# Optimization experiments

Measured on AMD Instinct MI355X. Metric: run time of the kernel, lower is better.

## Reference

```python
import jax, jax.numpy as jnp
import numpy as np

# --- config (matches init_kwargs) ---
E = 32          # n_routed_experts
G = 8           # n_group
TKG = 4         # topk_group
K = 4           # num_experts_per_tok
D = 2048        # hidden_size
H = 1024        # moe_intermediate_size
HS = 4096       # moe_shared_expert_intermediate_size
SCALE = 2.5     # routed_scaling_factor
CAP = 1024


def setup_inputs() -> dict:
    key = jax.random.key(0)
    ks = jax.random.split(key, 6)
    B, S = 2, 2048
    return dict(
        hidden_states=jax.random.normal(ks[0], (B, S, D), jnp.float32),
        gate_w=jax.random.normal(ks[1], (E, D), jnp.float32) * 0.02,
        bias_corr=jnp.zeros((E,), jnp.float32),  # e_score_correction_bias
        up_w=jax.random.normal(ks[2], (E, H, D), jnp.float32) * 0.02,
        down_w=jax.random.normal(ks[3], (E, D, H), jnp.float32) * 0.02,
        shared_up_w=jax.random.normal(ks[4], (HS, D), jnp.float32) * 0.02,
        shared_down_w=jax.random.normal(ks[5], (D, HS), jnp.float32) * 0.02,
    )


def relu2(x):
    r = jnp.maximum(x, 0.0)
    return r * r


def route_tokens(scores, bias_corr):
    # scores: sigmoid(router_logits), [T, E]
    T = scores.shape[0]
    scores_c = scores + bias_corr                                  # for choice
    group_scores = jax.lax.top_k(scores_c.reshape(T, G, E // G), 2)[0].sum(-1)  # [T, G]
    _, group_idx = jax.lax.top_k(group_scores, TKG)                # [T, TKG]
    group_mask = jnp.zeros((T, G), scores.dtype).at[jnp.arange(T)[:, None], group_idx].set(1.0)
    score_mask = jnp.repeat(group_mask, E // G, axis=1)            # [T, E]
    masked = jnp.where(score_mask > 0, scores_c, 0.0)
    _, topk_idx = jax.lax.top_k(masked, K)                         # [T, K]
    topk_w = jnp.take_along_axis(scores, topk_idx, axis=1)         # weights from raw sigmoid scores
    topk_w = topk_w / (topk_w.sum(-1, keepdims=True) + 1e-20)      # norm_topk_prob
    return topk_idx, topk_w * SCALE


def reference(hidden_states, gate_w, bias_corr, up_w, down_w, shared_up_w, shared_down_w):
    B, S, _ = hidden_states.shape
    T = B * S
    flat = hidden_states.reshape(T, D)

    logits = flat @ gate_w.T                                       # [T, E]
    scores = jax.nn.sigmoid(logits)
    topk_idx, topk_w = route_tokens(scores, bias_corr)             # [T, K] each

    # --- capacity-based dispatch (equivalent to per-expert gather + index_add combine) ---
    e_flat = topk_idx.reshape(-1)                                  # [T*K]
    oh = jax.nn.one_hot(e_flat, E, dtype=jnp.int32)                # [T*K, E]
    pos = jnp.take_along_axis(jnp.cumsum(oh, axis=0) - 1, e_flat[:, None], axis=1)[:, 0]
    tok = jnp.repeat(jnp.arange(T), K)                             # token idx per assignment
    valid = pos < CAP

    xe = jnp.zeros((E, CAP, D), flat.dtype).at[e_flat, pos].set(flat[tok], mode='drop')
    h = relu2(jnp.einsum('ecd,ehd->ech', xe, up_w))                # [E, CAP, H]
    ye = jnp.einsum('ech,edh->ecd', h, down_w)                     # [E, CAP, D]

    gathered = ye[e_flat, jnp.minimum(pos, CAP - 1)]               # [T*K, D]
    gathered = jnp.where(valid[:, None], gathered, 0.0) * topk_w.reshape(-1)[:, None]
    routed = gathered.reshape(T, K, D).sum(axis=1).reshape(B, S, D)

    shared = relu2(hidden_states @ shared_up_w.T) @ shared_down_w.T
    return routed + shared
```

## Files before the change

### kernel.cpp

```cpp
#include <hip/hip_runtime.h>

#define NE 32
#define NG 8
#define NK 4
#define ND 2048
#define NH 1024
#define NHS 4096
#define CAPE 1024
#define NT 4096

typedef float f32x4 __attribute__((ext_vector_type(4)));
typedef short s16x8 __attribute__((ext_vector_type(8)));

__device__ __forceinline__ short f2bf(float f) {
    return __builtin_bit_cast(short, (__bf16)f);
}
__device__ __forceinline__ float bf2f(short h) {
    return __builtin_bit_cast(float, ((unsigned)(unsigned short)h) << 16);
}

__device__ __forceinline__ void gload_lds16(const void* g, void* l) {
    __builtin_amdgcn_global_load_lds(
        (const __attribute__((address_space(1))) void*)g,
        (__attribute__((address_space(3))) void*)l, 16, 0, 0);
}

__global__ __launch_bounds__(256) void gate_kernel(
    const float* __restrict__ X, const float* __restrict__ Gw,
    const float* __restrict__ bias,
    int* __restrict__ topk_idx, float* __restrict__ topk_w)
{
    const int lane = threadIdx.x & 63;
    const int t = blockIdx.x * 4 + (threadIdx.x >> 6);
    const float* x = X + (size_t)t * ND;

    float xr[32];
#pragma unroll
    for (int i = 0; i < 32; i++) xr[i] = x[lane + i * 64];

    float scores[32];
#pragma unroll
    for (int e = 0; e < 32; e++) {
        const float* w = Gw + (size_t)e * ND;
        float a = 0.f;
#pragma unroll
        for (int i = 0; i < 32; i++) a = fmaf(xr[i], w[lane + i * 64], a);
#pragma unroll
        for (int s = 32; s > 0; s >>= 1) a += __shfl_xor(a, s);
        scores[e] = 1.0f / (1.0f + expf(-a));
    }

    float sc_c[32];
#pragma unroll
    for (int e = 0; e < 32; e++) sc_c[e] = scores[e] + bias[e];

    float gs[8];
#pragma unroll
    for (int g = 0; g < 8; g++) {
        float a = sc_c[4 * g], b = sc_c[4 * g + 1], c = sc_c[4 * g + 2], d = sc_c[4 * g + 3];
        float hi1 = fmaxf(a, b), lo1 = fminf(a, b);
        float hi2 = fmaxf(c, d), lo2 = fminf(c, d);
        float m1 = fmaxf(hi1, hi2);
        float m2 = fmaxf(fminf(hi1, hi2), fmaxf(lo1, lo2));
        gs[g] = m1 + m2;
    }

    unsigned gsel = 0;
#pragma unroll
    for (int it = 0; it < 4; it++) {
        int best = -1; float bv = -1e30f;
#pragma unroll
        for (int g = 0; g < 8; g++) {
            bool avail = !((gsel >> g) & 1);
            if (avail && gs[g] > bv) { bv = gs[g]; best = g; }
        }
        gsel |= 1u << best;
    }

    unsigned esel = 0;
    int idxs[4]; float wts[4];
#pragma unroll
    for (int it = 0; it < 4; it++) {
        int best = -1; float bv = -1e30f, braw = 0.f;
#pragma unroll
        for (int e = 0; e < 32; e++) {
            float mv = ((gsel >> (e >> 2)) & 1) ? sc_c[e] : 0.0f;
            bool avail = !((esel >> e) & 1);
            if (avail && mv > bv) { bv = mv; best = e; braw = scores[e]; }
        }
        esel |= 1u << best;
        idxs[it] = best; wts[it] = braw;
    }

    float s = wts[0] + wts[1] + wts[2] + wts[3] + 1e-20f;
    if (lane == 0) {
#pragma unroll
        for (int k = 0; k < 4; k++) {
            topk_idx[t * 4 + k] = idxs[k];
            topk_w[t * 4 + k] = wts[k] / s * 2.5f;
        }
    }
}

__global__ void zero_cnt(int* cnt) {
    if (threadIdx.x < NE) cnt[threadIdx.x] = 0;
}

__global__ void dispatch_kernel(const int* __restrict__ topk_idx,
                                int* __restrict__ cnt,
                                int* __restrict__ tok_list,
                                int* __restrict__ pos_list)
{
    int i = blockIdx.x * 256 + threadIdx.x;
    int e = topk_idx[i];
    int t = i >> 2;
    int pos = atomicAdd(&cnt[e], 1);
    pos_list[i] = pos;
    if (pos < CAPE) {
        tok_list[e * CAPE + pos] = t;
    }
}

__global__ __launch_bounds__(256) void cvt_f2bf(const float* __restrict__ in,
                                                short* __restrict__ out, int n8)
{
    int i = blockIdx.x * 256 + threadIdx.x;
    int stride = gridDim.x * 256;
    for (; i < n8; i += stride) {
        const f32x4* p = (const f32x4*)(in + (size_t)i * 8);
        f32x4 a = p[0], b = p[1];
        s16x8 h;
        h[0] = f2bf(a[0]); h[1] = f2bf(a[1]); h[2] = f2bf(a[2]); h[3] = f2bf(a[3]);
        h[4] = f2bf(b[0]); h[5] = f2bf(b[1]); h[6] = f2bf(b[2]); h[7] = f2bf(b[3]);
        *(s16x8*)(out + (size_t)i * 8) = h;
    }
}

__global__ __launch_bounds__(256) void combine_kernel(
    const int* __restrict__ topk_idx, const float* __restrict__ topk_w,
    const int* __restrict__ pos_list,
    const short* __restrict__ Ybuf, float* __restrict__ out)
{
    const int t = blockIdx.x;
    const int d0 = threadIdx.x * 8;

    int e[NK], p[NK]; float w[NK];
#pragma unroll
    for (int k = 0; k < NK; k++) {
        e[k] = topk_idx[t * NK + k];
        p[k] = pos_list[t * NK + k];
        w[k] = topk_w[t * NK + k];
    }

    float* orow = out + (size_t)t * ND + d0;
    f32x4 o0 = *(f32x4*)(orow);
    f32x4 o1 = *(f32x4*)(orow + 4);

#pragma unroll
    for (int k = 0; k < NK; k++) {
        if (p[k] < CAPE) {
            s16x8 y = *(const s16x8*)(Ybuf + ((size_t)e[k] * CAPE + p[k]) * ND + d0);
            o0[0] = fmaf(w[k], bf2f(y[0]), o0[0]);
            o0[1] = fmaf(w[k], bf2f(y[1]), o0[1]);
            o0[2] = fmaf(w[k], bf2f(y[2]), o0[2]);
            o0[3] = fmaf(w[k], bf2f(y[3]), o0[3]);
            o1[0] = fmaf(w[k], bf2f(y[4]), o1[0]);
            o1[1] = fmaf(w[k], bf2f(y[5]), o1[1]);
            o1[2] = fmaf(w[k], bf2f(y[6]), o1[2]);
            o1[3] = fmaf(w[k], bf2f(y[7]), o1[3]);
        }
    }
    *(f32x4*)(orow) = o0;
    *(f32x4*)(orow + 4) = o1;
}

template <int MODE>
__global__ __launch_bounds__(256, 2) void moe_gemm4(
    const short* __restrict__ Abase, const float* __restrict__ Bbase,
    const int* __restrict__ cnt, const int* __restrict__ tok_list,
    short* __restrict__ Hout, float* __restrict__ out)
{
    constexpr int K = (MODE == 0) ? ND : (MODE == 1) ? NH : (MODE == 2) ? ND : NHS;
    constexpr int NTILES = K / 64;

    const int e = blockIdx.z;
    const int m0 = blockIdx.y * 128, n0 = blockIdx.x * 128;

    int mcnt = 0;
    if constexpr (MODE == 0 || MODE == 1) {
        mcnt = min(cnt[e], CAPE);
        if (m0 >= mcnt) return;
    }

    __shared__ short As[2][128 * 64];
    __shared__ short Bs[2][128 * 64];

    const int tid = threadIdx.x;
    const int lane = tid & 63;
    const int wave = tid >> 6;
    const int wr = wave >> 1, wc = wave & 1;

    const short* Ab = Abase;
    const float* Bb = Bbase;
    if constexpr (MODE == 0) Bb += (size_t)e * NH * ND;
    if constexpr (MODE == 1) { Ab += (size_t)e * CAPE * NH; Bb += (size_t)e * ND * NH; }

    const int srow = tid >> 3;
    const int pA = tid & 7;
    const int gcolA = (pA ^ (srow & 7)) * 8;
    const short* asrc[4];
    int dstA[4];
#pragma unroll
    for (int o = 0; o < 4; o++) {
        int r = o * 32 + srow;
        if constexpr (MODE == 0) {
            int gr = min(m0 + r, mcnt - 1);
            int tok = tok_list[e * CAPE + gr];
            asrc[o] = Abase + (size_t)tok * ND + gcolA;
        } else if constexpr (MODE == 1) {
            int gr = min(m0 + r, mcnt - 1);
            asrc[o] = Ab + (size_t)gr * NH + gcolA;
        } else if constexpr (MODE == 2) {
            asrc[o] = Abase + (size_t)(m0 + r) * ND + gcolA;
        } else {
            asrc[o] = Abase + (size_t)(m0 + r) * NHS + gcolA;
        }
        dstA[o] = o * 2048 + wave * 512;
    }

    const int brow = tid >> 4;
    const int lc = tid & 15;
    const float* bsrc[8];
    int bdst[8];
#pragma unroll
    for (int o = 0; o < 8; o++) {
        int r = o * 16 + brow;
        bsrc[o] = Bb + (size_t)(n0 + r) * K + lc * 4;
        int ks = lc >> 1;
        bdst[o] = r * 64 + ((ks ^ (r & 7)) * 8) + (lc & 1) * 4;
    }

    auto STAGE_A = [&](int tt, int par) {
        const int ko = (tt < NTILES ? tt : NTILES - 1) * 64;
        short* Ad = As[par];
#pragma unroll
        for (int o = 0; o < 4; o++) gload_lds16(asrc[o] + ko, Ad + dstA[o]);
    };
    auto BLOAD = [&](int tt, f32x4* regs) {
        const int ko = (tt < NTILES ? tt : NTILES - 1) * 64;
#pragma unroll
        for (int o = 0; o < 8; o++) regs[o] = *(const f32x4*)(bsrc[o] + ko);
    };
    auto BWRITE = [&](const f32x4* regs, int par) {
        short* Bd = Bs[par];
#pragma unroll
        for (int o = 0; o < 8; o++) {
            short4 h;
            h.x = f2bf(regs[o][0]); h.y = f2bf(regs[o][1]);
            h.z = f2bf(regs[o][2]); h.w = f2bf(regs[o][3]);
            *(short4*)(Bd + bdst[o]) = h;
        }
    };

    const int r16 = lane & 15;
    const int physbase = ((lane >> 4) ^ (lane & 7)) * 8;
    int offA[4], offB[4];
#pragma unroll
    for (int m = 0; m < 4; m++)
        offA[m] = (wr * 64 + m * 16 + r16) * 64 + physbase;
#pragma unroll
    for (int n = 0; n < 4; n++)
        offB[n] = (wc * 64 + n * 16 + r16) * 64 + physbase;

    f32x4 acc[4][4] = {};
    f32x4 brE[8], brO[8];

    STAGE_A(0, 0); STAGE_A(1, 1);
    BLOAD(0, brE); BLOAD(1, brO);
    asm volatile("s_waitcnt vmcnt(8)" ::: "memory");
    __builtin_amdgcn_sched_barrier(0);
    BWRITE(brE, 0);
    asm volatile("s_waitcnt vmcnt(0)" ::: "memory");
    __builtin_amdgcn_sched_barrier(0);
    BWRITE(brO, 1);
    BLOAD(2, brE);
    asm volatile("s_waitcnt lgkmcnt(0)" ::: "memory");
    __builtin_amdgcn_sched_barrier(0);

#define GEMM_ITER(T, PAR, CONSUME, FILL)                                        \
    {                                                                           \
        __builtin_amdgcn_s_barrier();                                           \
        __builtin_amdgcn_sched_barrier(0);                                      \
        const short* At = As[PAR];                                              \
        const short* Bt = Bs[PAR];                                              \
        s16x8 af[4], bf[4];                                                     \
        _Pragma("unroll")                                                       \
        for (int m = 0; m < 4; m++) af[m] = *(const s16x8*)(At + offA[m]);      \
        _Pragma("unroll")                                                       \
        for (int n = 0; n < 4; n++) bf[n] = *(const s16x8*)(Bt + offB[n]);      \
        asm volatile("s_waitcnt lgkmcnt(0)" ::: "memory");                      \
        __builtin_amdgcn_sched_barrier(0);                                      \
        __builtin_amdgcn_s_setprio(1);                                          \
        _Pragma("unroll")                                                       \
        for (int m = 0; m < 4; m++)                                             \
            _Pragma("unroll")                                                   \
            for (int n = 0; n < 4; n++)                                         \
                acc[m][n] = __builtin_amdgcn_mfma_f32_16x16x32_bf16(            \
                    af[m], bf[n], acc[m][n], 0, 0, 0);                          \
        __builtin_amdgcn_s_setprio(0);                                          \
        s16x8 ag[4], bg[4];                                                     \
        _Pragma("unroll")                                                       \
        for (int m = 0; m < 4; m++) ag[m] = *(const s16x8*)(At + (offA[m] ^ 32)); \
        _Pragma("unroll")                                                       \
        for (int n = 0; n < 4; n++) bg[n] = *(const s16x8*)(Bt + (offB[n] ^ 32)); \
        asm volatile("s_waitcnt lgkmcnt(0)" ::: "memory");                      \
        __builtin_amdgcn_sched_barrier(0);                                      \
        __builtin_amdgcn_s_barrier();         \
        __builtin_amdgcn_sched_barrier(0);                                      \
        STAGE_A((T) + 2, PAR);                                                  \
        BLOAD((T) + 3, FILL);                                                   \
        asm volatile("s_waitcnt vmcnt(12)" ::: "memory");  \
        __builtin_amdgcn_sched_barrier(0);                                      \
        BWRITE(CONSUME, PAR);                                                   \
        __builtin_amdgcn_s_setprio(1);                                          \
        _Pragma("unroll")                                                       \
        for (int m = 0; m < 4; m++)                                             \
            _Pragma("unroll")                                                   \
            for (int n = 0; n < 4; n++)                                         \
                acc[m][n] = __builtin_amdgcn_mfma_f32_16x16x32_bf16(            \
                    ag[m], bg[n], acc[m][n], 0, 0, 0);                          \
        __builtin_amdgcn_s_setprio(0);                                          \
        asm volatile("s_waitcnt lgkmcnt(0)" ::: "memory");                      \
        __builtin_amdgcn_sched_barrier(0);                                      \
    }

    for (int t = 0; t < NTILES; t += 2) {
        GEMM_ITER(t,     0, brE, brO);
        GEMM_ITER(t + 1, 1, brO, brE);
    }
#undef GEMM_ITER

    const int r0 = (lane >> 4) * 4;
    const int cc = lane & 15;

    if constexpr (MODE == 0 || MODE == 2) {
#pragma unroll
        for (int i = 0; i < 4; i++)
#pragma unroll
            for (int j = 0; j < 4; j++)
#pragma unroll
                for (int v = 0; v < 4; v++) {
                    int row = wr * 64 + i * 16 + r0 + v;
                    int col = wc * 64 + j * 16 + cc;
                    float val = acc[i][j][v];
                    float r = fmaxf(val, 0.f);
                    val = r * r;
                    if constexpr (MODE == 0)
                        Hout[((size_t)e * CAPE + m0 + row) * NH + (n0 + col)] = f2bf(val);
                    else
                        Hout[(size_t)(m0 + row) * NHS + (n0 + col)] = f2bf(val);
                }
    } else if constexpr (MODE == 3) {
#pragma unroll
        for (int i = 0; i < 4; i++)
#pragma unroll
            for (int j = 0; j < 4; j++)
#pragma unroll
                for (int v = 0; v < 4; v++) {
                    int row = wr * 64 + i * 16 + r0 + v;
                    int col = wc * 64 + j * 16 + cc;
                    out[(size_t)(m0 + row) * ND + (n0 + col)] = acc[i][j][v];
                }
    } else {
#pragma unroll
        for (int i = 0; i < 4; i++)
#pragma unroll
            for (int v = 0; v < 4; v++) {
                int row = wr * 64 + i * 16 + r0 + v;
                int grow = m0 + row;
                if (grow < mcnt) {
#pragma unroll
                    for (int j = 0; j < 4; j++) {
                        int col = wc * 64 + j * 16 + cc;
                        Hout[((size_t)e * CAPE + grow) * ND + (n0 + col)] = f2bf(acc[i][j][v]);
                    }
                }
            }
    }
}

extern "C" void kernel_launch(void* const* d_in, const int* in_sizes, int n_in,
                              void* d_out, int out_size, void* d_ws, size_t ws_size,
                              hipStream_t stream) {
    const float* X    = (const float*)d_in[0];
    const float* Gw   = (const float*)d_in[1];
    const float* bias = (const float*)d_in[2];
    const float* up_w = (const float*)d_in[3];
    const float* dn_w = (const float*)d_in[4];
    const float* sup  = (const float*)d_in[5];
    const float* sdn  = (const float*)d_in[6];
    float* out = (float*)d_out;

    char* ws = (char*)d_ws;
    size_t off = 0;
    auto alloc = [&](size_t bytes) -> void* {
        off = (off + 255) & ~(size_t)255;
        void* p = ws + off;
        off += bytes;
        return p;
    };
    int*   cnt      = (int*)  alloc(NE * 4);
    int*   topk_idx = (int*)  alloc((size_t)NT * NK * 4);
    float* topk_w   = (float*)alloc((size_t)NT * NK * 4);
    int*   pos_list = (int*)  alloc((size_t)NT * NK * 4);
    int*   tok_list = (int*)  alloc((size_t)NE * CAPE * 4);
    short* Hbuf     = (short*)alloc((size_t)NE * CAPE * NH * 2);
    short* Sbuf     = (short*)alloc((size_t)NT * NHS * 2);
    short* Xbf      = (short*)alloc((size_t)NT * ND * 2);
    short* Ybuf     = (short*)alloc((size_t)NE * CAPE * ND * 2);

    gate_kernel<<<dim3(NT / 4), dim3(256), 0, stream>>>(X, Gw, bias, topk_idx, topk_w);
    zero_cnt<<<dim3(1), dim3(64), 0, stream>>>(cnt);
    dispatch_kernel<<<dim3(NT * NK / 256), dim3(256), 0, stream>>>(
        topk_idx, cnt, tok_list, pos_list);

    cvt_f2bf<<<dim3(1024), dim3(256), 0, stream>>>(X, Xbf, NT * ND / 8);

    moe_gemm4<0><<<dim3(NH / 128, CAPE / 128, NE), dim3(256), 0, stream>>>(
        Xbf, up_w, cnt, tok_list, Hbuf, nullptr);
    moe_gemm4<2><<<dim3(NHS / 128, NT / 128, 1), dim3(256), 0, stream>>>(
        Xbf, sup, nullptr, nullptr, Sbuf, nullptr);
    moe_gemm4<3><<<dim3(ND / 128, NT / 128, 1), dim3(256), 0, stream>>>(
        Sbuf, sdn, nullptr, nullptr, nullptr, out);
    moe_gemm4<1><<<dim3(ND / 128, CAPE / 128, NE), dim3(256), 0, stream>>>(
        Hbuf, dn_w, cnt, tok_list, Ybuf, nullptr);
    combine_kernel<<<dim3(NT), dim3(256), 0, stream>>>(
        topk_idx, topk_w, pos_list, Ybuf, out);
}
```

Baseline: 645.0 us.

## Restructure GEMM to K=32 tiles with 4-stage A pipeline and 3 blocks/CU

Rewrites the bf16 MFMA GEMM main loop to use 32-wide K tiles. A now streams through a 4-deep LDS ring and B is register-prefetched four tiles ahead and converted into a double-buffered LDS slot. Shrinking LDS per block and raising launch bounds to 3 blocks per SM is meant to increase occupancy and hide global load latency. The trade-off is twice as many barriers per K, fewer MFMAs between syncs, and added register pressure from four B register sets under a tighter VGPR budget.

Result: slower. 779.9 us (+20.9%).

```diff
diff --git a/kernel.cpp b/kernel.cpp
--- a/kernel.cpp
+++ b/kernel.cpp
@@ -175,13 +175,13 @@
 }
 
 template <int MODE>
-__global__ __launch_bounds__(256, 2) void moe_gemm4(
+__global__ __launch_bounds__(256, 3) void moe_gemm5(
     const short* __restrict__ Abase, const float* __restrict__ Bbase,
     const int* __restrict__ cnt, const int* __restrict__ tok_list,
     short* __restrict__ Hout, float* __restrict__ out)
 {
     constexpr int K = (MODE == 0) ? ND : (MODE == 1) ? NH : (MODE == 2) ? ND : NHS;
-    constexpr int NTILES = K / 64;
+    constexpr int NTILES = K / 32;
 
     const int e = blockIdx.z;
     const int m0 = blockIdx.y * 128, n0 = blockIdx.x * 128;
@@ -192,8 +192,8 @@
         if (m0 >= mcnt) return;
     }
 
-    __shared__ short As[2][128 * 64];
-    __shared__ short Bs[2][128 * 64];
+    __shared__ short As[4][128 * 32];
+    __shared__ short Bs[2][128 * 32];
 
     const int tid = threadIdx.x;
     const int lane = tid & 63;
@@ -205,14 +205,14 @@
     if constexpr (MODE == 0) Bb += (size_t)e * NH * ND;
     if constexpr (MODE == 1) { Ab += (size_t)e * CAPE * NH; Bb += (size_t)e * ND * NH; }
 
-    const int srow = tid >> 3;
-    const int pA = tid & 7;
-    const int gcolA = (pA ^ (srow & 7)) * 8;
-    const short* asrc[4];
-    int dstA[4];
-#pragma unroll
-    for (int o = 0; o < 4; o++) {
-        int r = o * 32 + srow;
+    const int arow = tid >> 2;
+    const int aslot = tid & 3;
+    const int gcolA = (aslot ^ (arow & 3)) * 8;
+    const short* asrc[2];
+    int dstA[2];
+#pragma unroll
+    for (int o = 0; o < 2; o++) {
+        int r = o * 64 + arow;
         if constexpr (MODE == 0) {
             int gr = min(m0 + r, mcnt - 1);
             int tok = tok_list[e * CAPE + gr];
@@ -228,71 +228,73 @@
         dstA[o] = o * 2048 + wave * 512;
     }
 
-    const int brow = tid >> 4;
-    const int lc = tid & 15;
-    const float* bsrc[8];
-    int bdst[8];
-#pragma unroll
-    for (int o = 0; o < 8; o++) {
-        int r = o * 16 + brow;
-        bsrc[o] = Bb + (size_t)(n0 + r) * K + lc * 4;
-        int ks = lc >> 1;
-        bdst[o] = r * 64 + ((ks ^ (r & 7)) * 8) + (lc & 1) * 4;
-    }
-
-    auto STAGE_A = [&](int tt, int par) {
-        const int ko = (tt < NTILES ? tt : NTILES - 1) * 64;
-        short* Ad = As[par];
-#pragma unroll
-        for (int o = 0; o < 4; o++) gload_lds16(asrc[o] + ko, Ad + dstA[o]);
+    const int brow = tid >> 1;
+    const int bhalf = tid & 1;
+    const float* bsrcp = Bb + (size_t)(n0 + brow) * K + bhalf * 16;
+    const int bd0 = brow * 32 + (((2 * bhalf)     ^ (brow & 3)) * 8);
+    const int bd1 = brow * 32 + (((2 * bhalf + 1) ^ (brow & 3)) * 8);
+
+    auto STAGE_A = [&](int tt) {
+        const int ko = (tt < NTILES ? tt : NTILES - 1) * 32;
+        short* Ad = As[tt & 3];
+#pragma unroll
+        for (int o = 0; o < 2; o++) gload_lds16(asrc[o] + ko, Ad + dstA[o]);
     };
     auto BLOAD = [&](int tt, f32x4* regs) {
-        const int ko = (tt < NTILES ? tt : NTILES - 1) * 64;
-#pragma unroll
-        for (int o = 0; o < 8; o++) regs[o] = *(const f32x4*)(bsrc[o] + ko);
+        const int ko = (tt < NTILES ? tt : NTILES - 1) * 32;
+#pragma unroll
+        for (int i = 0; i < 4; i++) regs[i] = *(const f32x4*)(bsrcp + ko + i * 4);
     };
     auto BWRITE = [&](const f32x4* regs, int par) {
         short* Bd = Bs[par];
-#pragma unroll
-        for (int o = 0; o < 8; o++) {
-            short4 h;
-            h.x = f2bf(regs[o][0]); h.y = f2bf(regs[o][1]);
-            h.z = f2bf(regs[o][2]); h.w = f2bf(regs[o][3]);
-            *(short4*)(Bd + bdst[o]) = h;
-        }
+        s16x8 h0, h1;
+        h0[0] = f2bf(regs[0][0]); h0[1] = f2bf(regs[0][1]);
+        h0[2] = f2bf(regs[0][2]); h0[3] = f2bf(regs[0][3]);
+        h0[4] = f2bf(regs[1][0]); h0[5] = f2bf(regs[1][1]);
+        h0[6] = f2bf(regs[1][2]); h0[7] = f2bf(regs[1][3]);
+        h1[0] = f2bf(regs[2][0]); h1[1] = f2bf(regs[2][1]);
+        h1[2] = f2bf(regs[2][2]); h1[3] = f2bf(regs[2][3]);
+        h1[4] = f2bf(regs[3][0]); h1[5] = f2bf(regs[3][1]);
+        h1[6] = f2bf(regs[3][2]); h1[7] = f2bf(regs[3][3]);
+        *(s16x8*)(Bd + bd0) = h0;
+        *(s16x8*)(Bd + bd1) = h1;
     };
 
     const int r16 = lane & 15;
-    const int physbase = ((lane >> 4) ^ (lane & 7)) * 8;
+    const int ks = lane >> 4;
+    const int physA = (ks ^ (r16 & 3)) * 8;
     int offA[4], offB[4];
 #pragma unroll
     for (int m = 0; m < 4; m++)
-        offA[m] = (wr * 64 + m * 16 + r16) * 64 + physbase;
+        offA[m] = (wr * 64 + m * 16 + r16) * 32 + physA;
 #pragma unroll
     for (int n = 0; n < 4; n++)
-        offB[n] = (wc * 64 + n * 16 + r16) * 64 + physbase;
+        offB[n] = (wc * 64 + n * 16 + r16) * 32 + physA;
 
     f32x4 acc[4][4] = {};
-    f32x4 brE[8], brO[8];
-
-    STAGE_A(0, 0); STAGE_A(1, 1);
-    BLOAD(0, brE); BLOAD(1, brO);
-    asm volatile("s_waitcnt vmcnt(8)" ::: "memory");
+    f32x4 br0[4], br1[4], br2[4], br3[4];
+
+    STAGE_A(0); BLOAD(0, br0);
+    BLOAD(1, br1); STAGE_A(1);
+    BLOAD(2, br2); STAGE_A(2);
+    BLOAD(3, br3);
+    asm volatile("s_waitcnt vmcnt(16)" ::: "memory");
     __builtin_amdgcn_sched_barrier(0);
-    BWRITE(brE, 0);
-    asm volatile("s_waitcnt vmcnt(0)" ::: "memory");
-    __builtin_amdgcn_sched_barrier(0);
-    BWRITE(brO, 1);
-    BLOAD(2, brE);
+    BWRITE(br0, 0);
     asm volatile("s_waitcnt lgkmcnt(0)" ::: "memory");
     __builtin_amdgcn_sched_barrier(0);
 
-#define GEMM_ITER(T, PAR, CONSUME, FILL)                                        \
+#define GEMM_ITER(T, BRW, BRL)                                                  \
     {                                                                           \
         __builtin_amdgcn_s_barrier();                                           \
         __builtin_amdgcn_sched_barrier(0);                                      \
-        const short* At = As[PAR];                                              \
-        const short* Bt = Bs[PAR];                                              \
+        STAGE_A((T) + 3);                                                       \
+        asm volatile("s_waitcnt vmcnt(12)" ::: "memory");                       \
+        __builtin_amdgcn_sched_barrier(0);                                      \
+        BWRITE(BRW, ((T) + 1) & 1);                                             \
+        BLOAD((T) + 4, BRL);                                                    \
+        const short* At = As[(T) & 3];                                          \
+        const short* Bt = Bs[(T) & 1];                                          \
         s16x8 af[4], bf[4];                                                     \
         _Pragma("unroll")                                                       \
         for (int m = 0; m < 4; m++) af[m] = *(const s16x8*)(At + offA[m]);      \
@@ -308,35 +310,13 @@
                 acc[m][n] = __builtin_amdgcn_mfma_f32_16x16x32_bf16(            \
                     af[m], bf[n], acc[m][n], 0, 0, 0);                          \
         __builtin_amdgcn_s_setprio(0);                                          \
-        s16x8 ag[4], bg[4];                                                     \
-        _Pragma("unroll")                                                       \
-        for (int m = 0; m < 4; m++) ag[m] = *(const s16x8*)(At + (offA[m] ^ 32)); \
-        _Pragma("unroll")                                                       \
-        for (int n = 0; n < 4; n++) bg[n] = *(const s16x8*)(Bt + (offB[n] ^ 32)); \
-        asm volatile("s_waitcnt lgkmcnt(0)" ::: "memory");                      \
-        __builtin_amdgcn_sched_barrier(0);                                      \
-        __builtin_amdgcn_s_barrier();         \
-        __builtin_amdgcn_sched_barrier(0);                                      \
-        STAGE_A((T) + 2, PAR);                                                  \
-        BLOAD((T) + 3, FILL);                                                   \
-        asm volatile("s_waitcnt vmcnt(12)" ::: "memory");  \
-        __builtin_amdgcn_sched_barrier(0);                                      \
-        BWRITE(CONSUME, PAR);                                                   \
-        __builtin_amdgcn_s_setprio(1);                                          \
-        _Pragma("unroll")                                                       \
-        for (int m = 0; m < 4; m++)                                             \
-            _Pragma("unroll")                                                   \
-            for (int n = 0; n < 4; n++)                                         \
-                acc[m][n] = __builtin_amdgcn_mfma_f32_16x16x32_bf16(            \
-                    ag[m], bg[n], acc[m][n], 0, 0, 0);                          \
-        __builtin_amdgcn_s_setprio(0);                                          \
-        asm volatile("s_waitcnt lgkmcnt(0)" ::: "memory");                      \
-        __builtin_amdgcn_sched_barrier(0);                                      \
-    }
-
-    for (int t = 0; t < NTILES; t += 2) {
-        GEMM_ITER(t,     0, brE, brO);
-        GEMM_ITER(t + 1, 1, brO, brE);
+    }
+
+    for (int t = 0; t < NTILES; t += 4) {
+        GEMM_ITER(t + 0, br1, br0);
+        GEMM_ITER(t + 1, br2, br1);
+        GEMM_ITER(t + 2, br3, br2);
+        GEMM_ITER(t + 3, br0, br3);
     }
 #undef GEMM_ITER
 
@@ -426,13 +406,13 @@
 
     cvt_f2bf<<<dim3(1024), dim3(256), 0, stream>>>(X, Xbf, NT * ND / 8);
 
-    moe_gemm4<0><<<dim3(NH / 128, CAPE / 128, NE), dim3(256), 0, stream>>>(
+    moe_gemm5<0><<<dim3(NH / 128, CAPE / 128, NE), dim3(256), 0, stream>>>(
         Xbf, up_w, cnt, tok_list, Hbuf, nullptr);
-    moe_gemm4<2><<<dim3(NHS / 128, NT / 128, 1), dim3(256), 0, stream>>>(
+    moe_gemm5<2><<<dim3(NHS / 128, NT / 128, 1), dim3(256), 0, stream>>>(
         Xbf, sup, nullptr, nullptr, Sbuf, nullptr);
-    moe_gemm4<3><<<dim3(ND / 128, NT / 128, 1), dim3(256), 0, stream>>>(
+    moe_gemm5<3><<<dim3(ND / 128, NT / 128, 1), dim3(256), 0, stream>>>(
         Sbuf, sdn, nullptr, nullptr, nullptr, out);
-    moe_gemm4<1><<<dim3(ND / 128, CAPE / 128, NE), dim3(256), 0, stream>>>(
+    moe_gemm5<1><<<dim3(ND / 128, CAPE / 128, NE), dim3(256), 0, stream>>>(
         Hbuf, dn_w, cnt, tok_list, Ybuf, nullptr);
     combine_kernel<<<dim3(NT), dim3(256), 0, stream>>>(
         topk_idx, topk_w, pos_list, Ybuf, out);
```

## Merge routed and shared GEMMs into combined up/down launches, fold counter zeroing

Applied to the files above, without the earlier changes.

Replaces the four templated GEMM launches with two grouped kernels: one runs the routed expert up-projections and the shared up-projection in a single grid, the other runs the routed and shared down-projections. The counter zeroing moves into the gate kernel, and the B-tile global load is issued at the start of each pipeline iteration instead of after the A staging. The intent is to cut launch count and tail idle time and to let shared-expert tiles fill CUs left empty by skipped routed tiles. In exchange, K and the routed/shared choice become runtime values, which may cost registers or unrolling, and the cnt reset relies on the gate kernel finishing before dispatch.

Measured after the change: 638.9 us, median of 3. About the same (-0.9%).

```diff
diff --git a/kernel.cpp b/kernel.cpp
--- a/kernel.cpp
+++ b/kernel.cpp
@@ -28,8 +28,11 @@
 __global__ __launch_bounds__(256) void gate_kernel(
     const float* __restrict__ X, const float* __restrict__ Gw,
     const float* __restrict__ bias,
-    int* __restrict__ topk_idx, float* __restrict__ topk_w)
+    int* __restrict__ topk_idx, float* __restrict__ topk_w,
+    int* __restrict__ cnt)
 {
+    if (blockIdx.x == 0 && threadIdx.x < NE) cnt[threadIdx.x] = 0;
+
     const int lane = threadIdx.x & 63;
     const int t = blockIdx.x * 4 + (threadIdx.x >> 6);
     const float* x = X + (size_t)t * ND;
@@ -100,10 +103,6 @@
             topk_w[t * 4 + k] = wts[k] / s * 2.5f;
         }
     }
-}
-
-__global__ void zero_cnt(int* cnt) {
-    if (threadIdx.x < NE) cnt[threadIdx.x] = 0;
 }
 
 __global__ void dispatch_kernel(const int* __restrict__ topk_idx,
@@ -174,123 +173,31 @@
     *(f32x4*)(orow + 4) = o1;
 }
 
-template <int MODE>
-__global__ __launch_bounds__(256, 2) void moe_gemm4(
-    const short* __restrict__ Abase, const float* __restrict__ Bbase,
-    const int* __restrict__ cnt, const int* __restrict__ tok_list,
-    short* __restrict__ Hout, float* __restrict__ out)
-{
-    constexpr int K = (MODE == 0) ? ND : (MODE == 1) ? NH : (MODE == 2) ? ND : NHS;
-    constexpr int NTILES = K / 64;
-
-    const int e = blockIdx.z;
-    const int m0 = blockIdx.y * 128, n0 = blockIdx.x * 128;
-
-    int mcnt = 0;
-    if constexpr (MODE == 0 || MODE == 1) {
-        mcnt = min(cnt[e], CAPE);
-        if (m0 >= mcnt) return;
-    }
-
-    __shared__ short As[2][128 * 64];
-    __shared__ short Bs[2][128 * 64];
-
-    const int tid = threadIdx.x;
-    const int lane = tid & 63;
-    const int wave = tid >> 6;
-    const int wr = wave >> 1, wc = wave & 1;
-
-    const short* Ab = Abase;
-    const float* Bb = Bbase;
-    if constexpr (MODE == 0) Bb += (size_t)e * NH * ND;
-    if constexpr (MODE == 1) { Ab += (size_t)e * CAPE * NH; Bb += (size_t)e * ND * NH; }
-
-    const int srow = tid >> 3;
-    const int pA = tid & 7;
-    const int gcolA = (pA ^ (srow & 7)) * 8;
-    const short* asrc[4];
-    int dstA[4];
-#pragma unroll
-    for (int o = 0; o < 4; o++) {
-        int r = o * 32 + srow;
-        if constexpr (MODE == 0) {
-            int gr = min(m0 + r, mcnt - 1);
-            int tok = tok_list[e * CAPE + gr];
-            asrc[o] = Abase + (size_t)tok * ND + gcolA;
-        } else if constexpr (MODE == 1) {
-            int gr = min(m0 + r, mcnt - 1);
-            asrc[o] = Ab + (size_t)gr * NH + gcolA;
-        } else if constexpr (MODE == 2) {
-            asrc[o] = Abase + (size_t)(m0 + r) * ND + gcolA;
-        } else {
-            asrc[o] = Abase + (size_t)(m0 + r) * NHS + gcolA;
-        }
-        dstA[o] = o * 2048 + wave * 512;
-    }
-
-    const int brow = tid >> 4;
-    const int lc = tid & 15;
-    const float* bsrc[8];
-    int bdst[8];
-#pragma unroll
-    for (int o = 0; o < 8; o++) {
-        int r = o * 16 + brow;
-        bsrc[o] = Bb + (size_t)(n0 + r) * K + lc * 4;
-        int ks = lc >> 1;
-        bdst[o] = r * 64 + ((ks ^ (r & 7)) * 8) + (lc & 1) * 4;
-    }
-
-    auto STAGE_A = [&](int tt, int par) {
-        const int ko = (tt < NTILES ? tt : NTILES - 1) * 64;
-        short* Ad = As[par];
-#pragma unroll
-        for (int o = 0; o < 4; o++) gload_lds16(asrc[o] + ko, Ad + dstA[o]);
-    };
-    auto BLOAD = [&](int tt, f32x4* regs) {
-        const int ko = (tt < NTILES ? tt : NTILES - 1) * 64;
-#pragma unroll
-        for (int o = 0; o < 8; o++) regs[o] = *(const f32x4*)(bsrc[o] + ko);
-    };
-    auto BWRITE = [&](const f32x4* regs, int par) {
-        short* Bd = Bs[par];
-#pragma unroll
-        for (int o = 0; o < 8; o++) {
-            short4 h;
-            h.x = f2bf(regs[o][0]); h.y = f2bf(regs[o][1]);
-            h.z = f2bf(regs[o][2]); h.w = f2bf(regs[o][3]);
-            *(short4*)(Bd + bdst[o]) = h;
-        }
-    };
-
-    const int r16 = lane & 15;
-    const int physbase = ((lane >> 4) ^ (lane & 7)) * 8;
-    int offA[4], offB[4];
-#pragma unroll
-    for (int m = 0; m < 4; m++)
-        offA[m] = (wr * 64 + m * 16 + r16) * 64 + physbase;
-#pragma unroll
-    for (int n = 0; n < 4; n++)
-        offB[n] = (wc * 64 + n * 16 + r16) * 64 + physbase;
-
-    f32x4 acc[4][4] = {};
-    f32x4 brE[8], brO[8];
-
-    STAGE_A(0, 0); STAGE_A(1, 1);
-    BLOAD(0, brE); BLOAD(1, brO);
-    asm volatile("s_waitcnt vmcnt(8)" ::: "memory");
-    __builtin_amdgcn_sched_barrier(0);
-    BWRITE(brE, 0);
-    asm volatile("s_waitcnt vmcnt(0)" ::: "memory");
-    __builtin_amdgcn_sched_barrier(0);
-    BWRITE(brO, 1);
-    BLOAD(2, brE);
-    asm volatile("s_waitcnt lgkmcnt(0)" ::: "memory");
-    __builtin_amdgcn_sched_barrier(0);
+#define GEMM_BODY_SETUP()                                                       \
+    __shared__ short As[2][128 * 64];                                           \
+    __shared__ short Bs[2][128 * 64];                                           \
+    const int tid = threadIdx.x;                                                \
+    const int lane = tid & 63;                                                  \
+    const int wave = tid >> 6;                                                  \
+    const int wr = wave >> 1, wc = wave & 1;                                    \
+    const int srow = tid >> 3;                                                  \
+    const int pA = tid & 7;                                                     \
+    const int gcolA = (pA ^ (srow & 7)) * 8;                                    \
+    const int brow = tid >> 4;                                                  \
+    const int lc = tid & 15;                                                    \
+    const int r16 = lane & 15;                                                  \
+    const int physbase = ((lane >> 4) ^ (lane & 7)) * 8;                        \
+    int offA[4], offB[4];                                                       \
+    _Pragma("unroll")                                                           \
+    for (int m = 0; m < 4; m++) offA[m] = (wr * 64 + m * 16 + r16) * 64 + physbase; \
+    _Pragma("unroll")                                                           \
+    for (int n = 0; n < 4; n++) offB[n] = (wc * 64 + n * 16 + r16) * 64 + physbase;
 
 #define GEMM_ITER(T, PAR, CONSUME, FILL)                                        \
     {                                                                           \
         __builtin_amdgcn_s_barrier();                                           \
         __builtin_amdgcn_sched_barrier(0);                                      \
+        BLOAD((T) + 3, FILL);                                                   \
         const short* At = As[PAR];                                              \
         const short* Bt = Bs[PAR];                                              \
         s16x8 af[4], bf[4];                                                     \
@@ -318,10 +225,9 @@
         __builtin_amdgcn_s_barrier();         \
         __builtin_amdgcn_sched_barrier(0);                                      \
         STAGE_A((T) + 2, PAR);                                                  \
-        BLOAD((T) + 3, FILL);                                                   \
         asm volatile("s_waitcnt vmcnt(12)" ::: "memory");  \
         __builtin_amdgcn_sched_barrier(0);                                      \
-        BWRITE(CONSUME, PAR);                                                   \
+        BWRITE(CONSUME, PAR);                            \
         __builtin_amdgcn_s_setprio(1);                                          \
         _Pragma("unroll")                                                       \
         for (int m = 0; m < 4; m++)                                             \
@@ -334,33 +240,227 @@
         __builtin_amdgcn_sched_barrier(0);                                      \
     }
 
+#define GEMM_PROLOGUE()                                                         \
+    STAGE_A(0, 0); STAGE_A(1, 1);                                               \
+    BLOAD(0, brE); BLOAD(1, brO);                                               \
+    asm volatile("s_waitcnt vmcnt(8)" ::: "memory");                            \
+    __builtin_amdgcn_sched_barrier(0);                                          \
+    BWRITE(brE, 0);                                                             \
+    asm volatile("s_waitcnt vmcnt(0)" ::: "memory");                            \
+    __builtin_amdgcn_sched_barrier(0);                                          \
+    BWRITE(brO, 1);                                                             \
+    BLOAD(2, brE);                                                              \
+    asm volatile("s_waitcnt lgkmcnt(0)" ::: "memory");                          \
+    __builtin_amdgcn_sched_barrier(0);
+
+__global__ __launch_bounds__(256, 2) void fused_up(
+    const short* __restrict__ Xbf, const float* __restrict__ up_w,
+    const float* __restrict__ sup,
+    const int* __restrict__ cnt, const int* __restrict__ tok_list,
+    short* __restrict__ Hbuf, short* __restrict__ Sbuf)
+{
+    constexpr int K = ND;
+    constexpr int NTILES = K / 64;
+
+    const int bid = blockIdx.x;
+    const bool routed = bid < 2048;
+    int e = 0, m0, n0, mcnt = 0;
+    const float* Bb;
+    if (routed) {
+        e = bid >> 6;
+        m0 = ((bid >> 3) & 7) * 128;
+        n0 = (bid & 7) * 128;
+        mcnt = min(cnt[e], CAPE);
+        if (m0 >= mcnt) return;
+        Bb = up_w + (size_t)e * NH * ND;
+    } else {
+        int lin = bid - 2048;
+        m0 = (lin >> 5) * 128;
+        n0 = (lin & 31) * 128;
+        Bb = sup;
+    }
+
+    GEMM_BODY_SETUP();
+
+    const short* asrc[4];
+    int dstA[4];
+#pragma unroll
+    for (int o = 0; o < 4; o++) {
+        int r = o * 32 + srow;
+        int arow;
+        if (routed) {
+            int gr = min(m0 + r, mcnt - 1);
+            arow = tok_list[e * CAPE + gr];
+        } else {
+            arow = m0 + r;
+        }
+        asrc[o] = Xbf + (size_t)arow * ND + gcolA;
+        dstA[o] = o * 2048 + wave * 512;
+    }
+
+    const float* bsrc[8];
+    int bdst[8];
+#pragma unroll
+    for (int o = 0; o < 8; o++) {
+        int r = o * 16 + brow;
+        bsrc[o] = Bb + (size_t)(n0 + r) * K + lc * 4;
+        int ks = lc >> 1;
+        bdst[o] = r * 64 + ((ks ^ (r & 7)) * 8) + (lc & 1) * 4;
+    }
+
+    auto STAGE_A = [&](int tt, int par) {
+        const int ko = (tt < NTILES ? tt : NTILES - 1) * 64;
+        short* Ad = As[par];
+#pragma unroll
+        for (int o = 0; o < 4; o++) gload_lds16(asrc[o] + ko, Ad + dstA[o]);
+    };
+    auto BLOAD = [&](int tt, f32x4* regs) {
+        const int ko = (tt < NTILES ? tt : NTILES - 1) * 64;
+#pragma unroll
+        for (int o = 0; o < 8; o++) regs[o] = *(const f32x4*)(bsrc[o] + ko);
+    };
+    auto BWRITE = [&](const f32x4* regs, int par) {
+        short* Bd = Bs[par];
+#pragma unroll
+        for (int o = 0; o < 8; o++) {
+            short4 h;
+            h.x = f2bf(regs[o][0]); h.y = f2bf(regs[o][1]);
+            h.z = f2bf(regs[o][2]); h.w = f2bf(regs[o][3]);
+            *(short4*)(Bd + bdst[o]) = h;
+        }
+    };
+
+    f32x4 acc[4][4] = {};
+    f32x4 brE[8], brO[8];
+
+    GEMM_PROLOGUE();
     for (int t = 0; t < NTILES; t += 2) {
         GEMM_ITER(t,     0, brE, brO);
         GEMM_ITER(t + 1, 1, brO, brE);
     }
-#undef GEMM_ITER
 
     const int r0 = (lane >> 4) * 4;
     const int cc = lane & 15;
-
-    if constexpr (MODE == 0 || MODE == 2) {
+#pragma unroll
+    for (int i = 0; i < 4; i++)
+#pragma unroll
+        for (int j = 0; j < 4; j++)
+#pragma unroll
+            for (int v = 0; v < 4; v++) {
+                int row = wr * 64 + i * 16 + r0 + v;
+                int col = wc * 64 + j * 16 + cc;
+                float val = acc[i][j][v];
+                float r = fmaxf(val, 0.f);
+                val = r * r;
+                if (routed)
+                    Hbuf[((size_t)e * CAPE + m0 + row) * NH + (n0 + col)] = f2bf(val);
+                else
+                    Sbuf[(size_t)(m0 + row) * NHS + (n0 + col)] = f2bf(val);
+            }
+}
+
+__global__ __launch_bounds__(256, 2) void fused_dn(
+    const short* __restrict__ Hbuf, const short* __restrict__ Sbuf,
+    const float* __restrict__ dn_w, const float* __restrict__ sdn,
+    const int* __restrict__ cnt, const int* __restrict__ tok_list,
+    short* __restrict__ Ybuf, float* __restrict__ out)
+{
+    const int bid = blockIdx.x;
+    const bool routed = bid < 4096;
+    int e = 0, m0, n0, mcnt = 0;
+    int K;
+    const short* Abase;
+    const float* Bb;
+    if (routed) {
+        e = bid >> 7;
+        m0 = ((bid >> 4) & 7) * 128;
+        n0 = (bid & 15) * 128;
+        mcnt = min(cnt[e], CAPE);
+        if (m0 >= mcnt) return;
+        K = NH;
+        Abase = Hbuf + (size_t)e * CAPE * NH;
+        Bb = dn_w + (size_t)e * ND * NH;
+    } else {
+        int lin = bid - 4096;
+        m0 = (lin >> 4) * 128;
+        n0 = (lin & 15) * 128;
+        K = NHS;
+        Abase = Sbuf;
+        Bb = sdn;
+    }
+    const int NTILES = K / 64;
+
+    GEMM_BODY_SETUP();
+
+    const short* asrc[4];
+    int dstA[4];
+#pragma unroll
+    for (int o = 0; o < 4; o++) {
+        int r = o * 32 + srow;
+        int arow = routed ? min(m0 + r, mcnt - 1) : (m0 + r);
+        asrc[o] = Abase + (size_t)arow * K + gcolA;
+        dstA[o] = o * 2048 + wave * 512;
+    }
+
+    const float* bsrc[8];
+    int bdst[8];
+#pragma unroll
+    for (int o = 0; o < 8; o++) {
+        int r = o * 16 + brow;
+        bsrc[o] = Bb + (size_t)(n0 + r) * K + lc * 4;
+        int ks = lc >> 1;
+        bdst[o] = r * 64 + ((ks ^ (r & 7)) * 8) + (lc & 1) * 4;
+    }
+
+    auto STAGE_A = [&](int tt, int par) {
+        const int ko = (tt < NTILES ? tt : NTILES - 1) * 64;
+        short* Ad = As[par];
+#pragma unroll
+        for (int o = 0; o < 4; o++) gload_lds16(asrc[o] + ko, Ad + dstA[o]);
+    };
+    auto BLOAD = [&](int tt, f32x4* regs) {
+        const int ko = (tt < NTILES ? tt : NTILES - 1) * 64;
+#pragma unroll
+        for (int o = 0; o < 8; o++) regs[o] = *(const f32x4*)(bsrc[o] + ko);
+    };
+    auto BWRITE = [&](const f32x4* regs, int par) {
+        short* Bd = Bs[par];
+#pragma unroll
+        for (int o = 0; o < 8; o++) {
+            short4 h;
+            h.x = f2bf(regs[o][0]); h.y = f2bf(regs[o][1]);
+            h.z = f2bf(regs[o][2]); h.w = f2bf(regs[o][3]);
+            *(short4*)(Bd + bdst[o]) = h;
+        }
+    };
+
+    f32x4 acc[4][4] = {};
+    f32x4 brE[8], brO[8];
+
+    GEMM_PROLOGUE();
+    for (int t = 0; t < NTILES; t += 2) {
+        GEMM_ITER(t,     0, brE, brO);
+        GEMM_ITER(t + 1, 1, brO, brE);
+    }
+
+    const int r0 = (lane >> 4) * 4;
+    const int cc = lane & 15;
+    if (routed) {
 #pragma unroll
         for (int i = 0; i < 4; i++)
 #pragma unroll
-            for (int j = 0; j < 4; j++)
-#pragma unroll
-                for (int v = 0; v < 4; v++) {
-                    int row = wr * 64 + i * 16 + r0 + v;
-                    int col = wc * 64 + j * 16 + cc;
-                    float val = acc[i][j][v];
-                    float r = fmaxf(val, 0.f);
-                    val = r * r;
-                    if constexpr (MODE == 0)
-                        Hout[((size_t)e * CAPE + m0 + row) * NH + (n0 + col)] = f2bf(val);
-                    else
-                        Hout[(size_t)(m0 + row) * NHS + (n0 + col)] = f2bf(val);
+            for (int v = 0; v < 4; v++) {
+                int row = wr * 64 + i * 16 + r0 + v;
+                int grow = m0 + row;
+                if (grow < mcnt) {
+#pragma unroll
+                    for (int j = 0; j < 4; j++) {
+                        int col = wc * 64 + j * 16 + cc;
+                        Ybuf[((size_t)e * CAPE + grow) * ND + (n0 + col)] = f2bf(acc[i][j][v]);
+                    }
                 }
-    } else if constexpr (MODE == 3) {
+            }
+    } else {
 #pragma unroll
         for (int i = 0; i < 4; i++)
 #pragma unroll
@@ -371,21 +471,6 @@
                     int col = wc * 64 + j * 16 + cc;
                     out[(size_t)(m0 + row) * ND + (n0 + col)] = acc[i][j][v];
                 }
-    } else {
-#pragma unroll
-        for (int i = 0; i < 4; i++)
-#pragma unroll
-            for (int v = 0; v < 4; v++) {
-                int row = wr * 64 + i * 16 + r0 + v;
-                int grow = m0 + row;
-                if (grow < mcnt) {
-#pragma unroll
-                    for (int j = 0; j < 4; j++) {
-                        int col = wc * 64 + j * 16 + cc;
-                        Hout[((size_t)e * CAPE + grow) * ND + (n0 + col)] = f2bf(acc[i][j][v]);
-                    }
-                }
-            }
     }
 }
 
@@ -419,21 +504,16 @@
     short* Xbf      = (short*)alloc((size_t)NT * ND * 2);
     short* Ybuf     = (short*)alloc((size_t)NE * CAPE * ND * 2);
 
-    gate_kernel<<<dim3(NT / 4), dim3(256), 0, stream>>>(X, Gw, bias, topk_idx, topk_w);
-    zero_cnt<<<dim3(1), dim3(64), 0, stream>>>(cnt);
+    gate_kernel<<<dim3(NT / 4), dim3(256), 0, stream>>>(X, Gw, bias, topk_idx, topk_w, cnt);
     dispatch_kernel<<<dim3(NT * NK / 256), dim3(256), 0, stream>>>(
         topk_idx, cnt, tok_list, pos_list);
 
     cvt_f2bf<<<dim3(1024), dim3(256), 0, stream>>>(X, Xbf, NT * ND / 8);
 
-    moe_gemm4<0><<<dim3(NH / 128, CAPE / 128, NE), dim3(256), 0, stream>>>(
-        Xbf, up_w, cnt, tok_list, Hbuf, nullptr);
-    moe_gemm4<2><<<dim3(NHS / 128, NT / 128, 1), dim3(256), 0, stream>>>(
-        Xbf, sup, nullptr, nullptr, Sbuf, nullptr);
-    moe_gemm4<3><<<dim3(ND / 128, NT / 128, 1), dim3(256), 0, stream>>>(
-        Sbuf, sdn, nullptr, nullptr, nullptr, out);
-    moe_gemm4<1><<<dim3(ND / 128, CAPE / 128, NE), dim3(256), 0, stream>>>(
-        Hbuf, dn_w, cnt, tok_list, Ybuf, nullptr);
+    fused_up<<<dim3(2048 + 1024), dim3(256), 0, stream>>>(
+        Xbf, up_w, sup, cnt, tok_list, Hbuf, Sbuf);
+    fused_dn<<<dim3(4096 + 512), dim3(256), 0, stream>>>(
+        Hbuf, Sbuf, dn_w, sdn, cnt, tok_list, Ybuf, out);
     combine_kernel<<<dim3(NT), dim3(256), 0, stream>>>(
         topk_idx, topk_w, pos_list, Ybuf, out);
 }
```
